# Performance work log

Hardware: AMD Instinct MI355X
Metric: run time of the kernel (lower is better)

Reference implementation:

```python
import jax, jax.numpy as jnp
import numpy as np

NUM_CLASSES = 8
ALPHA, GAMMA = 0.25, 2.0
EOS_COEF = 0.1
W_CE, W_BBOX, W_GIOU, W_CARD = 1.0, 5.0, 2.0, 1.0


def _build_empty_weight():
    class_counts = {0: 5158, 1: 102619, 2: 9545, 3: 9995, 4: 319, 5: 1128, 6: 729, 7: 2538}
    beta = 0.9999
    eff = {k: (1.0 - beta ** v) / (1.0 - beta) for k, v in class_counts.items()}
    total = sum(class_counts.values())
    inv = {k: total / v for k, v in class_counts.items()}
    mx = max(inv.values())
    ew = np.ones(NUM_CLASSES + 1, dtype=np.float32)
    for k in range(NUM_CLASSES):
        ew[k] = (inv[k] / mx) * (eff[4] / eff[k])
    ew[-1] = EOS_COEF
    return jnp.asarray(ew)


def setup_inputs() -> dict:
    key = jax.random.key(0)
    k1, k2, k3, k4, k5 = jax.random.split(key, 5)
    B, Q, C, Nt = 1024, 900, NUM_CLASSES, 32
    return {
        'pred_logits': jax.random.normal(k1, (B, Q, C), dtype=jnp.float32),
        'pred_boxes': jax.random.uniform(k2, (B, Q, 4), dtype=jnp.float32),
        'tgt_boxes': jax.random.uniform(k3, (B, Nt, 4), dtype=jnp.float32),
        'src_idx': jax.random.randint(k4, (B, Nt), 0, Q),
        'tgt_labels': jax.random.randint(k5, (B, Nt), 0, C),
        'empty_weight': _build_empty_weight(),
    }


def _cxcywh_to_xyxy(b):
    cx, cy, w, h = b[..., 0], b[..., 1], b[..., 2], b[..., 3]
    return jnp.stack([cx - 0.5 * w, cy - 0.5 * h, cx + 0.5 * w, cy + 0.5 * h], axis=-1)


def _paired_giou(a, b):
    # a, b: [N,4] xyxy; returns diag(generalized_box_iou(a,b)) without NxN matrix
    area_a = (a[:, 2] - a[:, 0]) * (a[:, 3] - a[:, 1])
    area_b = (b[:, 2] - b[:, 0]) * (b[:, 3] - b[:, 1])
    lt = jnp.maximum(a[:, :2], b[:, :2])
    rb = jnp.minimum(a[:, 2:], b[:, 2:])
    wh = jnp.clip(rb - lt, 0.0)
    inter = wh[:, 0] * wh[:, 1]
    union = area_a + area_b - inter
    iou = inter / union
    lt_e = jnp.minimum(a[:, :2], b[:, :2])
    rb_e = jnp.maximum(a[:, 2:], b[:, 2:])
    wh_e = jnp.clip(rb_e - lt_e, 0.0)
    area_e = wh_e[:, 0] * wh_e[:, 1]
    return iou - (area_e - union) / area_e


def reference(pred_logits, pred_boxes, tgt_boxes, src_idx, tgt_labels, empty_weight):
    B, Q, C = pred_logits.shape
    Nt = src_idx.shape[1]
    num_boxes = jnp.asarray(B * Nt, dtype=jnp.float32)
    bidx = jnp.arange(B)[:, None]

    # ---- labels: scatter matched labels, background = C ----
    target_classes = jnp.full((B, Q), C, dtype=jnp.int32).at[bidx, src_idx].set(tgt_labels.astype(jnp.int32))
    onehot = jax.nn.one_hot(target_classes, C, dtype=pred_logits.dtype)  # background -> all zeros
    # stable BCE-with-logits, elementwise focal
    bce = jnp.maximum(pred_logits, 0.0) - pred_logits * onehot + jnp.log1p(jnp.exp(-jnp.abs(pred_logits)))
    p = jax.nn.sigmoid(pred_logits)
    pt = jnp.where(onehot == 1.0, p, 1.0 - p)
    focal = jnp.where(onehot == 1.0, ALPHA, 1.0 - ALPHA) * (1.0 - pt) ** GAMMA * bce
    cls_w = empty_weight[jnp.clip(target_classes, 0, empty_weight.shape[0] - 1)]
    loss_ce = jnp.sum(focal * cls_w[..., None]) / (num_boxes + 1e-8)

    # ---- boxes: gather matched predictions ----
    src_boxes = pred_boxes[bidx, src_idx]            # [B,Nt,4]
    l1 = jnp.abs(src_boxes - tgt_boxes)
    rare = (tgt_labels == 4) | (tgt_labels == 5) | (tgt_labels == 6)
    scales = jnp.where(rare, 2.0, 1.0).astype(pred_boxes.dtype)  # [B,Nt]
    loss_bbox = jnp.sum(l1 * scales[..., None]) / (num_boxes + 1e-8)
    giou = _paired_giou(_cxcywh_to_xyxy(src_boxes.reshape(-1, 4)),
                        _cxcywh_to_xyxy(tgt_boxes.reshape(-1, 4)))
    loss_giou = jnp.sum((1.0 - giou) * scales.reshape(-1)) / (num_boxes + 1e-8)

    # ---- cardinality ----
    max_probs = jax.nn.sigmoid(pred_logits).max(axis=-1)
    card_pred = jnp.sum(max_probs > 0.5, axis=1).astype(jnp.float32)
    target_lengths = jnp.full((B,), Nt, dtype=jnp.float32)
    loss_card = jnp.mean(jnp.abs(card_pred - target_lengths))

    losses = jnp.stack([loss_ce, loss_bbox, loss_giou, loss_card])
    weights = jnp.asarray([W_CE, W_BBOX, W_GIOU, W_CARD], dtype=losses.dtype)
    return losses * weights
```

## Files before the change

kernel.cpp:

```cpp
#include <hip/hip_runtime.h>


constexpr int Bc  = 1024;
constexpr int Qc  = 900;
constexpr int Cc  = 8;
constexpr int NTc = 32;
constexpr int QH  = Qc / 2;
constexpr float kAlpha = 0.25f;

__device__ inline float wave_reduce(float v) {
#pragma unroll
    for (int o = 32; o > 0; o >>= 1) v += __shfl_down(v, o, 64);
    return v;
}

__global__ __launch_bounds__(256) void detr_main(
    const float* __restrict__ logits,
    const float* __restrict__ pboxes,
    const float* __restrict__ tboxes,
    const int*   __restrict__ sidx,
    const int*   __restrict__ tlbl,
    const float* __restrict__ ew,
    float4*      __restrict__ partials)
{
    const int blk  = blockIdx.x;
    const int b    = blk >> 1;
    const int half = blk & 1;
    const int tid  = threadIdx.x;

    __shared__ int   s_cls[Qc];
    __shared__ int   s_src[NTc];
    __shared__ int   s_lbl[NTc];
    __shared__ float s_ew[Cc + 1];
    __shared__ float s_red[4][4];

    for (int i = tid; i < Qc; i += 256) s_cls[i] = -1;
    if (tid < NTc) {
        s_src[tid] = sidx[b * NTc + tid];
        s_lbl[tid] = tlbl[b * NTc + tid];
    }
    if (tid < Cc + 1) s_ew[tid] = ew[tid];
    __syncthreads();
    if (tid < NTc) atomicMax(&s_cls[s_src[tid]], (tid << 8) | s_lbl[tid]);
    __syncthreads();

    const int qbase = half * QH;
    float ce = 0.f, card = 0.f;
    for (int qo = tid; qo < QH; qo += 256) {
        const int q = qbase + qo;
        const int packed = s_cls[q];
        const int tgt = (packed < 0) ? Cc : (packed & 0xFF);

        const float4* lp = (const float4*)(logits + ((size_t)(b * Qc + q)) * Cc);
        float4 xa = lp[0], xb = lp[1];
        float xs[8] = {xa.x, xa.y, xa.z, xa.w, xb.x, xb.y, xb.z, xb.w};

        float fs = 0.f, mx = -1e30f;
#pragma unroll
        for (int c = 0; c < Cc; ++c) {
            float x   = xs[c];
            mx        = fmaxf(mx, x);
            bool  oh  = (c == tgt);
            float e   = __expf(-fabsf(x));
            float l1p = __logf(1.f + e);
            float bce = fmaxf(x, 0.f) - (oh ? x : 0.f) + l1p;
            float inv = 1.f / (1.f + e);
            float p   = (x >= 0.f) ? inv : (1.f - inv);
            float pt  = oh ? p : (1.f - p);
            float om  = 1.f - pt;
            fs += (oh ? kAlpha : (1.f - kAlpha)) * om * om * bce;
        }
        ce   += fs * s_ew[tgt];
        card += (mx > 0.f) ? 1.f : 0.f;
    }

    float lbb = 0.f, lgi = 0.f;
    if (half == 0 && tid < NTc) {
        int q = s_src[tid], lab = s_lbl[tid];
        float4 sb = *(const float4*)(pboxes + ((size_t)(b * Qc + q)) * 4);
        float4 tb = *(const float4*)(tboxes + ((size_t)(b * NTc + tid)) * 4);
        float scale = (lab == 4 || lab == 5 || lab == 6) ? 2.f : 1.f;

        lbb = (fabsf(sb.x - tb.x) + fabsf(sb.y - tb.y) +
               fabsf(sb.z - tb.z) + fabsf(sb.w - tb.w)) * scale;

        float ax0 = sb.x - 0.5f * sb.z, ay0 = sb.y - 0.5f * sb.w;
        float ax1 = sb.x + 0.5f * sb.z, ay1 = sb.y + 0.5f * sb.w;
        float bx0 = tb.x - 0.5f * tb.z, by0 = tb.y - 0.5f * tb.w;
        float bx1 = tb.x + 0.5f * tb.z, by1 = tb.y + 0.5f * tb.w;

        float areaA = (ax1 - ax0) * (ay1 - ay0);
        float areaB = (bx1 - bx0) * (by1 - by0);
        float iw = fmaxf(fminf(ax1, bx1) - fmaxf(ax0, bx0), 0.f);
        float ih = fmaxf(fminf(ay1, by1) - fmaxf(ay0, by0), 0.f);
        float inter = iw * ih;
        float uni   = areaA + areaB - inter;
        float iou   = inter / uni;
        float ewd = fmaxf(fmaxf(ax1, bx1) - fminf(ax0, bx0), 0.f);
        float ehd = fmaxf(fmaxf(ay1, by1) - fminf(ay0, by0), 0.f);
        float areaE = ewd * ehd;
        float g = iou - (areaE - uni) / areaE;
        lgi = (1.f - g) * scale;
    }

    float vals[4] = {ce, lbb, lgi, card};
    const int lane = tid & 63, wave = tid >> 6;
#pragma unroll
    for (int k = 0; k < 4; ++k) {
        float v = wave_reduce(vals[k]);
        if (lane == 0) s_red[wave][k] = v;
    }
    __syncthreads();
    if (tid == 0) {
        float4 r;
        r.x = s_red[0][0] + s_red[1][0] + s_red[2][0] + s_red[3][0];
        r.y = s_red[0][1] + s_red[1][1] + s_red[2][1] + s_red[3][1];
        r.z = s_red[0][2] + s_red[1][2] + s_red[2][2] + s_red[3][2];
        r.w = s_red[0][3] + s_red[1][3] + s_red[2][3] + s_red[3][3];
        partials[blk] = r;
    }
}

__global__ __launch_bounds__(256) void detr_finalize(
    const float4* __restrict__ partials, float* __restrict__ out)
{
    const int tid = threadIdx.x;
    __shared__ float s_red[4][4];

    float4 a = {0.f, 0.f, 0.f, 0.f};
    for (int i = tid; i < Bc; i += 256) {
        float4 p0 = partials[2 * i];
        float4 p1 = partials[2 * i + 1];
        a.x += p0.x + p1.x;
        a.y += p0.y + p1.y;
        a.z += p0.z + p1.z;
        a.w += fabsf((p0.w + p1.w) - (float)NTc);
    }
    float vals[4] = {a.x, a.y, a.z, a.w};
    const int lane = tid & 63, wave = tid >> 6;
#pragma unroll
    for (int k = 0; k < 4; ++k) {
        float v = wave_reduce(vals[k]);
        if (lane == 0) s_red[wave][k] = v;
    }
    __syncthreads();
    if (tid == 0) {
        float ce   = s_red[0][0] + s_red[1][0] + s_red[2][0] + s_red[3][0];
        float bbox = s_red[0][1] + s_red[1][1] + s_red[2][1] + s_red[3][1];
        float giou = s_red[0][2] + s_red[1][2] + s_red[2][2] + s_red[3][2];
        float card = s_red[0][3] + s_red[1][3] + s_red[2][3] + s_red[3][3];
        const float nb = (float)(Bc * NTc) + 1e-8f;
        out[0] = 1.0f * ce   / nb;
        out[1] = 5.0f * bbox / nb;
        out[2] = 2.0f * giou / nb;
        out[3] = 1.0f * card / (float)Bc;
    }
}

extern "C" void kernel_launch(void* const* d_in, const int* in_sizes, int n_in,
                              void* d_out, int out_size, void* d_ws, size_t ws_size,
                              hipStream_t stream) {
    const float* logits = (const float*)d_in[0];
    const float* pboxes = (const float*)d_in[1];
    const float* tboxes = (const float*)d_in[2];
    const int*   sidx   = (const int*)d_in[3];
    const int*   tlbl   = (const int*)d_in[4];
    const float* ew     = (const float*)d_in[5];
    float4* partials = (float4*)d_ws;

    detr_main<<<2 * Bc, 256, 0, stream>>>(logits, pboxes, tboxes, sidx, tlbl, ew, partials);
    detr_finalize<<<1, 256, 0, stream>>>(partials, (float*)d_out);
}
```

Measured before the change: 97.14 us.

## Fuse finalize into main kernel via atomics with one 512-thread block per batch

Drops the separate finalize kernel and workspace partials. Each block now covers one whole batch item with 512 threads and atomically adds its scaled contributions straight into the output, which is zeroed first by a memset. This trades the second kernel launch and the per-block partial writes for 4096 global float atomics on four addresses, a memset launch, and a result that depends on summation order.

```diff
diff --git a/kernel.cpp b/kernel.cpp
--- a/kernel.cpp
+++ b/kernel.cpp
@@ -5,7 +5,6 @@
 constexpr int Qc  = 900;
 constexpr int Cc  = 8;
 constexpr int NTc = 32;
-constexpr int QH  = Qc / 2;
 constexpr float kAlpha = 0.25f;
 
 __device__ inline float wave_reduce(float v) {
@@ -14,27 +13,25 @@
     return v;
 }
 
-__global__ __launch_bounds__(256) void detr_main(
+__global__ __launch_bounds__(512) void detr_main(
     const float* __restrict__ logits,
     const float* __restrict__ pboxes,
     const float* __restrict__ tboxes,
     const int*   __restrict__ sidx,
     const int*   __restrict__ tlbl,
     const float* __restrict__ ew,
-    float4*      __restrict__ partials)
+    float*       __restrict__ out)
 {
-    const int blk  = blockIdx.x;
-    const int b    = blk >> 1;
-    const int half = blk & 1;
-    const int tid  = threadIdx.x;
+    const int b   = blockIdx.x;
+    const int tid = threadIdx.x;
 
     __shared__ int   s_cls[Qc];
     __shared__ int   s_src[NTc];
     __shared__ int   s_lbl[NTc];
     __shared__ float s_ew[Cc + 1];
-    __shared__ float s_red[4][4];
+    __shared__ float s_red[8][4];
 
-    for (int i = tid; i < Qc; i += 256) s_cls[i] = -1;
+    for (int i = tid; i < Qc; i += 512) s_cls[i] = -1;
     if (tid < NTc) {
         s_src[tid] = sidx[b * NTc + tid];
         s_lbl[tid] = tlbl[b * NTc + tid];
@@ -44,10 +41,8 @@
     if (tid < NTc) atomicMax(&s_cls[s_src[tid]], (tid << 8) | s_lbl[tid]);
     __syncthreads();
 
-    const int qbase = half * QH;
     float ce = 0.f, card = 0.f;
-    for (int qo = tid; qo < QH; qo += 256) {
-        const int q = qbase + qo;
+    for (int q = tid; q < Qc; q += 512) {
         const int packed = s_cls[q];
         const int tgt = (packed < 0) ? Cc : (packed & 0xFF);
 
@@ -75,7 +70,7 @@
     }
 
     float lbb = 0.f, lgi = 0.f;
-    if (half == 0 && tid < NTc) {
+    if (tid < NTc) {
         int q = s_src[tid], lab = s_lbl[tid];
         float4 sb = *(const float4*)(pboxes + ((size_t)(b * Qc + q)) * 4);
         float4 tb = *(const float4*)(tboxes + ((size_t)(b * NTc + tid)) * 4);
@@ -112,48 +107,19 @@
     }
     __syncthreads();
     if (tid == 0) {
-        float4 r;
-        r.x = s_red[0][0] + s_red[1][0] + s_red[2][0] + s_red[3][0];
-        r.y = s_red[0][1] + s_red[1][1] + s_red[2][1] + s_red[3][1];
-        r.z = s_red[0][2] + s_red[1][2] + s_red[2][2] + s_red[3][2];
-        r.w = s_red[0][3] + s_red[1][3] + s_red[2][3] + s_red[3][3];
-        partials[blk] = r;
-    }
-}
-
-__global__ __launch_bounds__(256) void detr_finalize(
-    const float4* __restrict__ partials, float* __restrict__ out)
-{
-    const int tid = threadIdx.x;
-    __shared__ float s_red[4][4];
-
-    float4 a = {0.f, 0.f, 0.f, 0.f};
-    for (int i = tid; i < Bc; i += 256) {
-        float4 p0 = partials[2 * i];
-        float4 p1 = partials[2 * i + 1];
-        a.x += p0.x + p1.x;
-        a.y += p0.y + p1.y;
-        a.z += p0.z + p1.z;
-        a.w += fabsf((p0.w + p1.w) - (float)NTc);
-    }
-    float vals[4] = {a.x, a.y, a.z, a.w};
-    const int lane = tid & 63, wave = tid >> 6;
+        float s[4];
 #pragma unroll
-    for (int k = 0; k < 4; ++k) {
-        float v = wave_reduce(vals[k]);
-        if (lane == 0) s_red[wave][k] = v;
-    }
-    __syncthreads();
-    if (tid == 0) {
-        float ce   = s_red[0][0] + s_red[1][0] + s_red[2][0] + s_red[3][0];
-        float bbox = s_red[0][1] + s_red[1][1] + s_red[2][1] + s_red[3][1];
-        float giou = s_red[0][2] + s_red[1][2] + s_red[2][2] + s_red[3][2];
-        float card = s_red[0][3] + s_red[1][3] + s_red[2][3] + s_red[3][3];
+        for (int k = 0; k < 4; ++k) {
+            float a = 0.f;
+#pragma unroll
+            for (int w = 0; w < 8; ++w) a += s_red[w][k];
+            s[k] = a;
+        }
         const float nb = (float)(Bc * NTc) + 1e-8f;
-        out[0] = 1.0f * ce   / nb;
-        out[1] = 5.0f * bbox / nb;
-        out[2] = 2.0f * giou / nb;
-        out[3] = 1.0f * card / (float)Bc;
+        atomicAdd(&out[0], 1.0f * s[0] / nb);
+        atomicAdd(&out[1], 5.0f * s[1] / nb);
+        atomicAdd(&out[2], 2.0f * s[2] / nb);
+        atomicAdd(&out[3], fabsf(s[3] - (float)NTc) / (float)Bc);
     }
 }
 
@@ -166,8 +132,8 @@
     const int*   sidx   = (const int*)d_in[3];
     const int*   tlbl   = (const int*)d_in[4];
     const float* ew     = (const float*)d_in[5];
-    float4* partials = (float4*)d_ws;
+    float* out = (float*)d_out;
 
-    detr_main<<<2 * Bc, 256, 0, stream>>>(logits, pboxes, tboxes, sidx, tlbl, ew, partials);
-    detr_finalize<<<1, 256, 0, stream>>>(partials, (float*)d_out);
+    hipMemsetAsync(out, 0, (size_t)out_size * sizeof(float), stream);
+    detr_main<<<Bc, 512, 0, stream>>>(logits, pboxes, tboxes, sidx, tlbl, ew, out);
 }
```

Measured after the change: 139.5 us. 1.44x slower.
